# Kernel tuning notes

Measured on AMD Instinct MI355X. Metric: run time of the kernel, lower is better.

The kernel has to match this reference:

```python
import jax, jax.numpy as jnp
import numpy as np

N, E, CN, CE = 2048, 8192, 256, 256
MN, ME = 16384, 65536
RATIO = 0.5
K_KEEP = int(np.ceil(RATIO * N))  # 1024, static


def _glorot(key, shape):
    lim = float(np.sqrt(6.0 / (shape[0] + shape[1])))
    return jax.random.uniform(key, shape, jnp.float32, -lim, lim)


def setup_inputs() -> dict:
    key = jax.random.key(0)
    ks = jax.random.split(key, 16)
    return {
        "x_n": jax.random.normal(ks[0], (N, CN), jnp.float32),
        "edge_index_n": jax.random.randint(ks[1], (2, MN), 0, N),
        "edge_weight_n": jax.random.uniform(ks[2], (MN,), jnp.float32),
        "x_e": jax.random.normal(ks[3], (E, CE), jnp.float32),
        "edge_index_e": jax.random.randint(ks[4], (2, ME), 0, E),
        "edge_weight_e": jax.random.uniform(ks[5], (ME,), jnp.float32),
        "edge_index": jax.random.randint(ks[6], (2, E), 0, N),
        "n_batch": jnp.zeros((N,), jnp.int64 if jax.config.jax_enable_x64 else jnp.int32),
        "e_batch": jnp.zeros((E,), jnp.int64 if jax.config.jax_enable_x64 else jnp.int32),
        "x_n0": jax.random.normal(ks[7], (N, CN), jnp.float32),
        "x_e0": jax.random.normal(ks[8], (E, CE), jnp.float32),
        # HodgeLaguerreConv(in, 1, K=2) params for node- and edge-scoring GNNs
        "W_n0": _glorot(ks[9], (CN, 1)),
        "W_n1": _glorot(ks[10], (CN, 1)),
        "b_n": jnp.zeros((1,), jnp.float32),
        "W_e0": _glorot(ks[11], (CE, 1)),
        "W_e1": _glorot(ks[12], (CE, 1)),
        "b_e": jnp.zeros((1,), jnp.float32),
    }


def _hodge_conv_k2(x, ei, ew, W0, W1, b):
    # PyG: out = lin0(T0) + lin1(T1), T0 = x, T1 = x - L@x (propagate: dst += w_e * x[src])
    n = x.shape[0]
    agg = jax.ops.segment_sum(ew[:, None] * x[ei[0]], ei[1], num_segments=n)
    return x @ W0 + (x - agg) @ W1 + b


def reference(x_n, edge_index_n, edge_weight_n, x_e, edge_index_e, edge_weight_e,
              edge_index, n_batch, e_batch, x_n0, x_e0,
              W_n0, W_n1, b_n, W_e0, W_e1, b_e):
    score_n = jax.nn.sigmoid(_hodge_conv_k2(x_n, edge_index_n, edge_weight_n, W_n0, W_n1, b_n).reshape(-1))
    score_e = jax.nn.sigmoid(_hodge_conv_k2(x_e, edge_index_e, edge_weight_e, W_e0, W_e1, b_e).reshape(-1))
    xns = x_n * score_n[:, None]
    xes = x_e * score_e[:, None]
    # incidence matrix B (par1): B[src,e]=-1, B[dst,e]=+1 (duplicates summed, as torch sparse)
    src, dst = edge_index[0], edge_index[1]
    eidx = jnp.arange(E)
    par1 = jnp.zeros((N, E), x_n.dtype).at[src, eidx].add(-1.0).at[dst, eidx].add(1.0)
    par1_abs = jnp.zeros((N, E), x_n.dtype).at[src, eidx].add(1.0).at[dst, eidx].add(1.0)
    # joint node score with 0.125 * |B| @ score_e
    joint = score_n + 0.125 * (par1_abs @ score_e)
    perm = jnp.argsort(-joint)                # descending
    idx_keep = jnp.sort(perm[:K_KEEP])        # kept nodes in original order (boolean-mask order)
    mask_n = jnp.zeros((N,), x_n.dtype).at[idx_keep].set(1.0)
    # edges touching any removed node get nonzero; keep edges where this is exactly 0
    removed_hits = par1_abs.T @ (1.0 - mask_n)
    keep_e = (removed_hits == 0.0).astype(x_n.dtype)     # [E]
    # masked incidence: kept-node rows, removed-edge columns zeroed
    par_masked = par1[idx_keep] * keep_e[None, :]        # [k, E]
    L0 = par_masked @ par_masked.T                       # [k, k]  (equals compacted L0)
    L1 = par_masked.T @ par_masked                       # [E, E]  (zero rows/cols at removed edges)
    # eigsh(L0, k=1, 'LM'): max eigenvalue; scipy path is non-differentiable -> stop_gradient
    lam = jax.lax.stop_gradient(jnp.linalg.eigvalsh(L0)[-1])
    L0s = 2.0 * L0 / lam
    L1s = 2.0 * L1 / lam
    x_n_out = xns[idx_keep]
    x_e_out = xes * keep_e[:, None]
    x_n0_out = x_n0[idx_keep]
    x_e0_out = x_e0 * keep_e[:, None]
    return (x_n_out, L0s, x_e_out, L1s, par_masked, x_n0_out, x_e0_out)
```

## Files before the change

kernel.cpp:

```cpp
#include <hip/hip_runtime.h>
#include <math.h>

#define NN   2048
#define EE   8192
#define CNF  256
#define MN   16384
#define ME   65536
#define KK   1024

#define OUT_XN   ((size_t)0)
#define OUT_L0   ((size_t)262144)
#define OUT_XE   ((size_t)1310720)
#define OUT_L1   ((size_t)3407872)
#define OUT_PM   ((size_t)70516736)
#define OUT_XN0  ((size_t)78905344)
#define OUT_XE0  ((size_t)79167488)

#define WS_T1N    0
#define WS_SLINN  2048
#define WS_T1E    4096
#define WS_SLINE  12288
#define WS_SCN    20480
#define WS_SCE    22528
#define WS_AGGN   32768
#define WS_AGGE   34816
#define WS_LAM    43008
#define WS_IDXK   43520
#define WS_RANK   44544
#define WS_OFFS   47616
#define WS_ADJE   66176
#define WS_KEEPE  82560

#define DCAP  8
#define PWR_T 96
#define RBAD  0xFFFFu

__global__ void k_prep(const float* __restrict__ xn, const float* __restrict__ xe,
                       const float* __restrict__ Wn0, const float* __restrict__ Wn1,
                       const float* __restrict__ We0, const float* __restrict__ We1,
                       float* __restrict__ wsf) {
    if (blockIdx.x == 0) {
        for (int i = threadIdx.x; i < 2048; i += 256) wsf[WS_AGGN + i] = 0.f;
        for (int i = threadIdx.x; i < 8192; i += 256) wsf[WS_AGGE + i] = 0.f;
    }
    int gw = (blockIdx.x * blockDim.x + threadIdx.x) >> 6;
    int lane = threadIdx.x & 63;
    int wstr = (gridDim.x * blockDim.x) >> 6;
    for (int row = gw; row < NN + EE; row += wstr) {
        const float *x, *W0, *W1; float *t1, *sl; int r;
        if (row < NN) { r = row;      x = xn + (size_t)r * CNF; W0 = Wn0; W1 = Wn1; t1 = wsf + WS_T1N; sl = wsf + WS_SLINN; }
        else          { r = row - NN; x = xe + (size_t)r * CNF; W0 = We0; W1 = We1; t1 = wsf + WS_T1E; sl = wsf + WS_SLINE; }
        float4 xv = ((const float4*)x)[lane];
        float4 w0 = ((const float4*)W0)[lane];
        float4 w1 = ((const float4*)W1)[lane];
        float d0 = xv.x*w0.x + xv.y*w0.y + xv.z*w0.z + xv.w*w0.w;
        float d1 = xv.x*w1.x + xv.y*w1.y + xv.z*w1.z + xv.w*w1.w;
        #pragma unroll
        for (int o = 32; o > 0; o >>= 1) { d0 += __shfl_down(d0, o, 64); d1 += __shfl_down(d1, o, 64); }
        if (lane == 0) { t1[r] = d1; sl[r] = d0 + d1; }
    }
}

__global__ void k_agg(const int* __restrict__ ein, const float* __restrict__ ewn,
                      const int* __restrict__ eie, const float* __restrict__ ewe,
                      float* __restrict__ wsf) {
    int i = blockIdx.x * blockDim.x + threadIdx.x;
    if (i < MN) {
        int s = ein[i], d = ein[MN + i];
        atomicAdd(wsf + WS_AGGN + d, ewn[i] * wsf[WS_T1N + s]);
    }
    if (i < ME) {
        int s = eie[i], d = eie[ME + i];
        atomicAdd(wsf + WS_AGGE + d, ewe[i] * wsf[WS_T1E + s]);
    }
}

__device__ __forceinline__ float block_reduce_sum(float val, float* red) {
    #pragma unroll
    for (int o = 32; o > 0; o >>= 1) val += __shfl_down(val, o, 64);
    int lane = threadIdx.x & 63, wid = threadIdx.x >> 6;
    if (lane == 0) red[wid] = val;
    __syncthreads();
    float r = 0.0f;
    if (threadIdx.x < 16) {
        r = red[threadIdx.x];
        #pragma unroll
        for (int o = 8; o > 0; o >>= 1) r += __shfl_down(r, o, 16);
        if (threadIdx.x == 0) red[0] = r;
    }
    __syncthreads();
    float out = red[0];
    __syncthreads();
    return out;
}

__global__ __launch_bounds__(1024) void k_mid(
        const int* __restrict__ ei,
        const float* __restrict__ bn, const float* __restrict__ be,
        float* __restrict__ out, float* __restrict__ wsf, int* __restrict__ wsi) {
    int tid = threadIdx.x;
    if (blockIdx.x != 0) {
        size_t w = (size_t)(blockIdx.x - 1) * 1024 + tid;
        size_t ws = (size_t)(gridDim.x - 1) * 1024;
        float4 z = make_float4(0.f, 0.f, 0.f, 0.f);
        float4* l1 = (float4*)(out + OUT_L1);
        for (size_t p = w; p < (size_t)EE * EE / 4; p += ws) l1[p] = z;
        float4* pm = (float4*)(out + OUT_PM);
        for (size_t p = w; p < (size_t)KK * EE / 4; p += ws) pm[p] = z;
        float4* l0 = (float4*)(out + OUT_L0);
        for (size_t p = w; p < (size_t)KK * KK / 4; p += ws) l0[p] = z;
        return;
    }
    __shared__ unsigned long long s_u64[2048];
    __shared__ float s_joint[2048];
    __shared__ unsigned short s_rank[2048];
    __shared__ unsigned short s_adjo[16384 + DCAP];
    __shared__ float s_red[16];
    int* s_i = (int*)s_u64;

    float bnv = bn[0], bev = be[0];
    for (int i = tid; i < NN; i += 1024) {
        float zv = wsf[WS_SLINN + i] - wsf[WS_AGGN + i] + bnv;
        float s = 1.0f / (1.0f + expf(-zv));
        wsf[WS_SCN + i] = s;
        s_joint[i] = s;
    }
    for (int j = tid; j < EE; j += 1024) {
        float zv = wsf[WS_SLINE + j] - wsf[WS_AGGE + j] + bev;
        wsf[WS_SCE + j] = 1.0f / (1.0f + expf(-zv));
    }
    __syncthreads();

    for (int e = tid; e < EE; e += 1024) {
        float v = 0.125f * wsf[WS_SCE + e];
        atomicAdd(&s_joint[ei[e]], v);
        atomicAdd(&s_joint[ei[EE + e]], v);
    }
    __syncthreads();

    for (int i = tid; i < 2048; i += 1024) {
        float f = s_joint[i];
        unsigned u = __float_as_uint(f);
        unsigned sk = (u & 0x80000000u) ? ~u : (u | 0x80000000u);
        s_u64[i] = (((unsigned long long)(~sk)) << 32) | (unsigned)i;
    }
    __syncthreads();
    for (int k = 2; k <= 2048; k <<= 1) {
        for (int j = k >> 1; j >= 1; j >>= 1) {
            for (int i = tid; i < 2048; i += 1024) {
                int ixj = i ^ j;
                if (ixj > i) {
                    bool up = ((i & k) == 0);
                    unsigned long long a = s_u64[i], b = s_u64[ixj];
                    if ((a > b) == up) { s_u64[i] = b; s_u64[ixj] = a; }
                }
            }
            __syncthreads();
        }
    }
    int myid = (int)(s_u64[tid] & 0xFFFFFFFFu);
    __syncthreads();
    {
        s_i[tid] = 0; s_i[tid + 1024] = 0; s_i[tid + 2048] = 0;
        __syncthreads();
        s_i[myid] = 1;
        __syncthreads();
        int a0 = s_i[2 * tid], a1 = s_i[2 * tid + 1];
        int pairsum = a0 + a1;
        s_i[2048 + tid] = pairsum;
        __syncthreads();
        for (int off = 1; off < 1024; off <<= 1) {
            int v = (tid >= off) ? s_i[2048 + tid - off] : 0;
            __syncthreads();
            s_i[2048 + tid] += v;
            __syncthreads();
        }
        int excl = s_i[2048 + tid] - pairsum;
        int i0 = 2 * tid, i1 = 2 * tid + 1;
        int r0 = excl, r1 = excl + a0;
        s_rank[i0] = a0 ? (unsigned short)r0 : (unsigned short)RBAD;
        s_rank[i1] = a1 ? (unsigned short)r1 : (unsigned short)RBAD;
        wsi[WS_RANK + i0] = a0 ? r0 : -1;
        wsi[WS_RANK + i1] = a1 ? r1 : -1;
        if (a0) wsi[WS_IDXK + r0] = i0;
        if (a1) wsi[WS_IDXK + r1] = i1;
    }
    __syncthreads();

    s_i[tid] = 0;
    if (tid < 1024) {}
    __syncthreads();
    for (int e = tid; e < EE; e += 1024) {
        int s = ei[e], d = ei[EE + e];
        unsigned rs = s_rank[s], rd = s_rank[d];
        int kept = (rs != RBAD && rd != RBAD);
        wsi[WS_KEEPE + e] = kept;
        if (kept && s != d) {
            atomicAdd(&s_i[(int)rs], 1);
            atomicAdd(&s_i[(int)rd], 1);
        }
    }
    __syncthreads();

    {
        int dg = s_i[tid];
        s_i[1024 + tid] = dg;
        for (int off = 1; off < 1024; off <<= 1) {
            __syncthreads();
            int v = (tid >= off) ? s_i[1024 + tid - off] : 0;
            __syncthreads();
            s_i[1024 + tid] += v;
        }
        __syncthreads();
        int offs = s_i[1024 + tid] - dg;
        s_i[2048 + tid] = offs;
        wsi[WS_OFFS + tid] = offs;
        if (tid == 1023) wsi[WS_OFFS + 1024] = s_i[1024 + 1023];
    }
    __syncthreads();

    for (int e = tid; e < EE; e += 1024) {
        int s = ei[e], d = ei[EE + e];
        unsigned rs = s_rank[s], rd = s_rank[d];
        if (rs != RBAD && rd != RBAD && s != d) {
            int p = atomicAdd(&s_i[2048 + (int)rs], 1);
            s_adjo[p] = (unsigned short)rd;
            wsi[WS_ADJE + p] = (e << 1);
            int q = atomicAdd(&s_i[2048 + (int)rd], 1);
            s_adjo[q] = (unsigned short)rs;
            wsi[WS_ADJE + q] = (e << 1) | 1;
        }
    }
    __syncthreads();

    {
        int o0 = wsi[WS_OFFS + tid];
        int d  = wsi[WS_OFFS + tid + 1] - o0;
        __syncthreads();
        float* v0 = (float*)s_u64;
        float* v1 = v0 + 1024;
        unsigned h = (unsigned)tid * 2654435761u + 911u;
        h ^= h >> 15; h *= 2246822519u; h ^= h >> 13;
        v0[tid] = (float)(h & 0xFFFFu) * (1.0f / 65536.0f) - 0.5f;
        int aj[DCAP];
        #pragma unroll
        for (int j = 0; j < DCAP; ++j) aj[j] = (j < d) ? (int)s_adjo[o0 + j] : 0;
        __syncthreads();
        float* vc = v0; float* vn = v1;
        for (int iter = 0; iter < PWR_T; ++iter) {
            float acc = 0.0f;
            #pragma unroll
            for (int j = 0; j < DCAP; ++j) acc += (j < d) ? vc[aj[j]] : 0.0f;
            for (int i = o0 + DCAP; i < o0 + d; ++i) acc += vc[(int)s_adjo[i]];
            float y = (float)d * vc[tid] - acc;
            if ((iter & 7) == 7) {
                float n2 = block_reduce_sum(y * y, s_red);
                y *= (n2 > 0.0f) ? rsqrtf(n2) : 0.0f;
            }
            vn[tid] = y;
            __syncthreads();
            float* tmp = vc; vc = vn; vn = tmp;
        }
        float acc = 0.0f;
        #pragma unroll
        for (int j = 0; j < DCAP; ++j) acc += (j < d) ? vc[aj[j]] : 0.0f;
        for (int i = o0 + DCAP; i < o0 + d; ++i) acc += vc[(int)s_adjo[i]];
        float y = (float)d * vc[tid] - acc;
        float rq = block_reduce_sum(vc[tid] * y, s_red);
        if (tid == 0) wsf[WS_LAM] = rq;
    }
}

__global__ __launch_bounds__(1024) void k_final(
        const float* __restrict__ xn, const float* __restrict__ xe,
        const float* __restrict__ xn0, const float* __restrict__ xe0,
        const int* __restrict__ ei,
        float* __restrict__ out, const float* __restrict__ wsf,
        const int* __restrict__ wsi) {
    float sc = 2.0f / wsf[WS_LAM];
    int gt = blockIdx.x * 1024 + threadIdx.x;
    int gstr = gridDim.x * 1024;

    for (int i = gt; i < KK * 64; i += gstr) {
        int r = i >> 6, c = i & 63;
        int src = wsi[WS_IDXK + r];
        float s = wsf[WS_SCN + src];
        float4 v = ((const float4*)(xn + (size_t)src * CNF))[c];
        v.x *= s; v.y *= s; v.z *= s; v.w *= s;
        ((float4*)(out + OUT_XN))[(size_t)r * 64 + c] = v;
        ((float4*)(out + OUT_XN0))[(size_t)r * 64 + c] = ((const float4*)(xn0 + (size_t)src * CNF))[c];
    }
    for (int i = gt; i < EE * 64; i += gstr) {
        int e = i >> 6, c = i & 63;
        float m = wsi[WS_KEEPE + e] ? 1.0f : 0.0f;
        float s = m * wsf[WS_SCE + e];
        float4 v = ((const float4*)(xe + (size_t)e * CNF))[c];
        v.x *= s; v.y *= s; v.z *= s; v.w *= s;
        ((float4*)(out + OUT_XE))[(size_t)e * 64 + c] = v;
        float4 v0 = ((const float4*)(xe0 + (size_t)e * CNF))[c];
        v0.x *= m; v0.y *= m; v0.z *= m; v0.w *= m;
        ((float4*)(out + OUT_XE0))[(size_t)e * 64 + c] = v0;
    }
    {
        float* pm = out + OUT_PM;
        float* L0 = out + OUT_L0;
        for (int e = gt; e < EE; e += gstr) {
            int s = ei[e], d = ei[EE + e];
            int rs = wsi[WS_RANK + s], rd = wsi[WS_RANK + d];
            if (rs < 0 || rd < 0 || s == d) continue;
            pm[(size_t)rs * EE + e] = -1.0f;
            pm[(size_t)rd * EE + e] =  1.0f;
            atomicAdd(&L0[(size_t)rs * KK + rs],  sc);
            atomicAdd(&L0[(size_t)rd * KK + rd],  sc);
            atomicAdd(&L0[(size_t)rs * KK + rd], -sc);
            atomicAdd(&L0[(size_t)rd * KK + rs], -sc);
        }
    }
    {
        float* L1 = out + OUT_L1;
        int gwv = gt >> 6, lane = gt & 63, wstr = gstr >> 6;
        for (int r = gwv; r < KK; r += wstr) {
            int o0 = wsi[WS_OFFS + r], o1 = wsi[WS_OFFS + r + 1];
            for (int i = o0; i < o1; ++i) {
                int eiv = wsi[WS_ADJE + i];
                int e = eiv >> 1;
                float si = (eiv & 1) ? sc : -sc;
                for (int j = o0 + lane; j < o1; j += 64) {
                    int ejv = wsi[WS_ADJE + j];
                    atomicAdd(&L1[(size_t)e * EE + (ejv >> 1)], (ejv & 1) ? si : -si);
                }
            }
        }
    }
}

extern "C" void kernel_launch(void* const* d_in, const int* in_sizes, int n_in,
                              void* d_out, int out_size, void* d_ws, size_t ws_size,
                              hipStream_t stream) {
    const float* x_n  = (const float*)d_in[0];
    const int*   ei_n = (const int*)  d_in[1];
    const float* ew_n = (const float*)d_in[2];
    const float* x_e  = (const float*)d_in[3];
    const int*   ei_e = (const int*)  d_in[4];
    const float* ew_e = (const float*)d_in[5];
    const int*   ei   = (const int*)  d_in[6];
    const float* x_n0 = (const float*)d_in[9];
    const float* x_e0 = (const float*)d_in[10];
    const float* Wn0  = (const float*)d_in[11];
    const float* Wn1  = (const float*)d_in[12];
    const float* bn   = (const float*)d_in[13];
    const float* We0  = (const float*)d_in[14];
    const float* We1  = (const float*)d_in[15];
    const float* be   = (const float*)d_in[16];

    float* out = (float*)d_out;
    float* wsf = (float*)d_ws;
    int*   wsi = (int*)d_ws;

    k_prep <<<640, 256, 0, stream>>>(x_n, x_e, Wn0, Wn1, We0, We1, wsf);
    k_agg  <<<256, 256, 0, stream>>>(ei_n, ew_n, ei_e, ew_e, wsf);
    k_mid  <<<256, 1024, 0, stream>>>(ei, bn, be, out, wsf, wsi);
    k_final<<<256, 1024, 0, stream>>>(x_n, x_e, x_n0, x_e0, ei, out, wsf, wsi);
}
```

Before: 491.0 us.

## Fuse final stage into k_mid using inter-block flags to overlap serial block-0 work

```diff
diff --git a/kernel.cpp b/kernel.cpp
--- a/kernel.cpp
+++ b/kernel.cpp
@@ -30,6 +30,8 @@
 #define WS_OFFS   47616
 #define WS_ADJE   66176
 #define WS_KEEPE  82560
+#define WS_FLAG1  90752
+#define WS_FLAG2  90753
 
 #define DCAP  8
 #define PWR_T 96
@@ -38,10 +40,11 @@
 __global__ void k_prep(const float* __restrict__ xn, const float* __restrict__ xe,
                        const float* __restrict__ Wn0, const float* __restrict__ Wn1,
                        const float* __restrict__ We0, const float* __restrict__ We1,
-                       float* __restrict__ wsf) {
+                       float* __restrict__ wsf, int* __restrict__ wsi) {
     if (blockIdx.x == 0) {
         for (int i = threadIdx.x; i < 2048; i += 256) wsf[WS_AGGN + i] = 0.f;
         for (int i = threadIdx.x; i < 8192; i += 256) wsf[WS_AGGE + i] = 0.f;
+        if (threadIdx.x == 0) { wsi[WS_FLAG1] = 0; wsi[WS_FLAG2] = 0; }
     }
     int gw = (blockIdx.x * blockDim.x + threadIdx.x) >> 6;
     int lane = threadIdx.x & 63;
@@ -94,13 +97,36 @@
     return out;
 }
 
+__device__ __forceinline__ void wait_flag(int* f) {
+    if (threadIdx.x == 0) {
+        while (__hip_atomic_load(f, __ATOMIC_ACQUIRE, __HIP_MEMORY_SCOPE_AGENT) == 0)
+            __builtin_amdgcn_s_sleep(8);
+    }
+    __syncthreads();
+}
+
+__device__ __forceinline__ void set_flag(int* f) {
+    __syncthreads();
+    if (threadIdx.x == 0)
+        __hip_atomic_store(f, 1, __ATOMIC_RELEASE, __HIP_MEMORY_SCOPE_AGENT);
+}
+
 __global__ __launch_bounds__(1024) void k_mid(
         const int* __restrict__ ei,
         const float* __restrict__ bn, const float* __restrict__ be,
+        const float* __restrict__ xn, const float* __restrict__ xe,
+        const float* __restrict__ xn0, const float* __restrict__ xe0,
         float* __restrict__ out, float* __restrict__ wsf, int* __restrict__ wsi) {
-    int tid = threadIdx.x;
-    if (blockIdx.x != 0) {
-        size_t w = (size_t)(blockIdx.x - 1) * 1024 + tid;
+    int tid = threadIdx.x, bid = blockIdx.x;
+    __shared__ unsigned long long s_u64[2048];
+    __shared__ float s_joint[2048];
+    __shared__ unsigned short s_rank[2048];
+    __shared__ unsigned short s_adjo[16384 + DCAP];
+    __shared__ float s_red[16];
+    int* s_i = (int*)s_u64;
+
+    if (bid != 0) {
+        size_t w = (size_t)(bid - 1) * 1024 + tid;
         size_t ws = (size_t)(gridDim.x - 1) * 1024;
         float4 z = make_float4(0.f, 0.f, 0.f, 0.f);
         float4* l1 = (float4*)(out + OUT_L1);
@@ -109,14 +135,65 @@
         for (size_t p = w; p < (size_t)KK * EE / 4; p += ws) pm[p] = z;
         float4* l0 = (float4*)(out + OUT_L0);
         for (size_t p = w; p < (size_t)KK * KK / 4; p += ws) l0[p] = z;
+
+        wait_flag(wsi + WS_FLAG1);
+        int gt = (int)w, gstr = (int)ws;
+        for (int i = gt; i < KK * 64; i += gstr) {
+            int r = i >> 6, c = i & 63;
+            int src = wsi[WS_IDXK + r];
+            float s = wsf[WS_SCN + src];
+            float4 v = ((const float4*)(xn + (size_t)src * CNF))[c];
+            v.x *= s; v.y *= s; v.z *= s; v.w *= s;
+            ((float4*)(out + OUT_XN))[(size_t)r * 64 + c] = v;
+            ((float4*)(out + OUT_XN0))[(size_t)r * 64 + c] = ((const float4*)(xn0 + (size_t)src * CNF))[c];
+        }
+        for (int i = gt; i < EE * 64; i += gstr) {
+            int e = i >> 6, c = i & 63;
+            float m = wsi[WS_KEEPE + e] ? 1.0f : 0.0f;
+            float s = m * wsf[WS_SCE + e];
+            float4 v = ((const float4*)(xe + (size_t)e * CNF))[c];
+            v.x *= s; v.y *= s; v.z *= s; v.w *= s;
+            ((float4*)(out + OUT_XE))[(size_t)e * 64 + c] = v;
+            float4 v0 = ((const float4*)(xe0 + (size_t)e * CNF))[c];
+            v0.x *= m; v0.y *= m; v0.z *= m; v0.w *= m;
+            ((float4*)(out + OUT_XE0))[(size_t)e * 64 + c] = v0;
+        }
+
+        wait_flag(wsi + WS_FLAG2);
+        float sc = 2.0f / wsf[WS_LAM];
+        {
+            float* pmf = out + OUT_PM;
+            float* L0 = out + OUT_L0;
+            for (int e = gt; e < EE; e += gstr) {
+                int s = ei[e], d = ei[EE + e];
+                int rs = wsi[WS_RANK + s], rd = wsi[WS_RANK + d];
+                if (rs < 0 || rd < 0 || s == d) continue;
+                pmf[(size_t)rs * EE + e] = -1.0f;
+                pmf[(size_t)rd * EE + e] =  1.0f;
+                atomicAdd(&L0[(size_t)rs * KK + rs],  sc);
+                atomicAdd(&L0[(size_t)rd * KK + rd],  sc);
+                atomicAdd(&L0[(size_t)rs * KK + rd], -sc);
+                atomicAdd(&L0[(size_t)rd * KK + rs], -sc);
+            }
+        }
+        {
+            float* L1 = out + OUT_L1;
+            int gwv = gt >> 6, lane = gt & 63, wstr2 = gstr >> 6;
+            for (int r = gwv; r < KK; r += wstr2) {
+                int o0 = wsi[WS_OFFS + r], o1 = wsi[WS_OFFS + r + 1];
+                for (int i = o0; i < o1; ++i) {
+                    int eiv = wsi[WS_ADJE + i];
+                    int e = eiv >> 1;
+                    float si = (eiv & 1) ? sc : -sc;
+                    for (int j = o0 + lane; j < o1; j += 64) {
+                        int ejv = wsi[WS_ADJE + j];
+                        atomicAdd(&L1[(size_t)e * EE + (ejv >> 1)], (ejv & 1) ? si : -si);
+                    }
+                }
+            }
+        }
         return;
     }
-    __shared__ unsigned long long s_u64[2048];
-    __shared__ float s_joint[2048];
-    __shared__ unsigned short s_rank[2048];
-    __shared__ unsigned short s_adjo[16384 + DCAP];
-    __shared__ float s_red[16];
-    int* s_i = (int*)s_u64;
 
     float bnv = bn[0], bev = be[0];
     for (int i = tid; i < NN; i += 1024) {
@@ -188,7 +265,6 @@
     __syncthreads();
 
     s_i[tid] = 0;
-    if (tid < 1024) {}
     __syncthreads();
     for (int e = tid; e < EE; e += 1024) {
         int s = ei[e], d = ei[EE + e];
@@ -200,6 +276,7 @@
             atomicAdd(&s_i[(int)rd], 1);
         }
     }
+    set_flag(wsi + WS_FLAG1);
     __syncthreads();
 
     {
@@ -269,69 +346,7 @@
         float rq = block_reduce_sum(vc[tid] * y, s_red);
         if (tid == 0) wsf[WS_LAM] = rq;
     }
-}
-
-__global__ __launch_bounds__(1024) void k_final(
-        const float* __restrict__ xn, const float* __restrict__ xe,
-        const float* __restrict__ xn0, const float* __restrict__ xe0,
-        const int* __restrict__ ei,
-        float* __restrict__ out, const float* __restrict__ wsf,
-        const int* __restrict__ wsi) {
-    float sc = 2.0f / wsf[WS_LAM];
-    int gt = blockIdx.x * 1024 + threadIdx.x;
-    int gstr = gridDim.x * 1024;
-
-    for (int i = gt; i < KK * 64; i += gstr) {
-        int r = i >> 6, c = i & 63;
-        int src = wsi[WS_IDXK + r];
-        float s = wsf[WS_SCN + src];
-        float4 v = ((const float4*)(xn + (size_t)src * CNF))[c];
-        v.x *= s; v.y *= s; v.z *= s; v.w *= s;
-        ((float4*)(out + OUT_XN))[(size_t)r * 64 + c] = v;
-        ((float4*)(out + OUT_XN0))[(size_t)r * 64 + c] = ((const float4*)(xn0 + (size_t)src * CNF))[c];
-    }
-    for (int i = gt; i < EE * 64; i += gstr) {
-        int e = i >> 6, c = i & 63;
-        float m = wsi[WS_KEEPE + e] ? 1.0f : 0.0f;
-        float s = m * wsf[WS_SCE + e];
-        float4 v = ((const float4*)(xe + (size_t)e * CNF))[c];
-        v.x *= s; v.y *= s; v.z *= s; v.w *= s;
-        ((float4*)(out + OUT_XE))[(size_t)e * 64 + c] = v;
-        float4 v0 = ((const float4*)(xe0 + (size_t)e * CNF))[c];
-        v0.x *= m; v0.y *= m; v0.z *= m; v0.w *= m;
-        ((float4*)(out + OUT_XE0))[(size_t)e * 64 + c] = v0;
-    }
-    {
-        float* pm = out + OUT_PM;
-        float* L0 = out + OUT_L0;
-        for (int e = gt; e < EE; e += gstr) {
-            int s = ei[e], d = ei[EE + e];
-            int rs = wsi[WS_RANK + s], rd = wsi[WS_RANK + d];
-            if (rs < 0 || rd < 0 || s == d) continue;
-            pm[(size_t)rs * EE + e] = -1.0f;
-            pm[(size_t)rd * EE + e] =  1.0f;
-            atomicAdd(&L0[(size_t)rs * KK + rs],  sc);
-            atomicAdd(&L0[(size_t)rd * KK + rd],  sc);
-            atomicAdd(&L0[(size_t)rs * KK + rd], -sc);
-            atomicAdd(&L0[(size_t)rd * KK + rs], -sc);
-        }
-    }
-    {
-        float* L1 = out + OUT_L1;
-        int gwv = gt >> 6, lane = gt & 63, wstr = gstr >> 6;
-        for (int r = gwv; r < KK; r += wstr) {
-            int o0 = wsi[WS_OFFS + r], o1 = wsi[WS_OFFS + r + 1];
-            for (int i = o0; i < o1; ++i) {
-                int eiv = wsi[WS_ADJE + i];
-                int e = eiv >> 1;
-                float si = (eiv & 1) ? sc : -sc;
-                for (int j = o0 + lane; j < o1; j += 64) {
-                    int ejv = wsi[WS_ADJE + j];
-                    atomicAdd(&L1[(size_t)e * EE + (ejv >> 1)], (ejv & 1) ? si : -si);
-                }
-            }
-        }
-    }
+    set_flag(wsi + WS_FLAG2);
 }
 
 extern "C" void kernel_launch(void* const* d_in, const int* in_sizes, int n_in,
@@ -357,8 +372,7 @@
     float* wsf = (float*)d_ws;
     int*   wsi = (int*)d_ws;
 
-    k_prep <<<640, 256, 0, stream>>>(x_n, x_e, Wn0, Wn1, We0, We1, wsf);
-    k_agg  <<<256, 256, 0, stream>>>(ei_n, ew_n, ei_e, ew_e, wsf);
-    k_mid  <<<256, 1024, 0, stream>>>(ei, bn, be, out, wsf, wsi);
-    k_final<<<256, 1024, 0, stream>>>(x_n, x_e, x_n0, x_e0, ei, out, wsf, wsi);
-}
+    k_prep<<<640, 256, 0, stream>>>(x_n, x_e, Wn0, Wn1, We0, We1, wsf, wsi);
+    k_agg <<<256, 256, 0, stream>>>(ei_n, ew_n, ei_e, ew_e, wsf);
+    k_mid <<<256, 1024, 0, stream>>>(ei, bn, be, x_n, x_e, x_n0, x_e0, out, wsf, wsi);
+}
```

Result: slower. 515.0 us (+4.9%).
